# Kernel tuning notes

Hardware: AMD Instinct MI355X
Metric: run time of the kernel (lower is better)

## Reference

```python
import jax, jax.numpy as jnp
import numpy as np

B = 1048576  # batch size
EPS_CLAMP_LO = 1e-6
EPS_CLAMP_HI = 1.0 - 1e-6


def _build_mask():
    # mask[k, i, j] = 1 iff i + j == k, flattened to [19, 100]
    i = np.arange(10)
    m = np.zeros((19, 10, 10), dtype=np.float32)
    ii, jj = np.meshgrid(i, i, indexing='ij')
    m[(ii + jj).ravel(), ii.ravel(), jj.ravel()] = 1.0
    return jnp.asarray(m.reshape(19, 100))


def setup_inputs() -> dict:
    key = jax.random.key(0)
    k1, k2, k3, k4 = jax.random.split(key, 4)
    # concept probabilities: uniform then normalize rows to sum 1
    p1 = jax.random.uniform(k1, (B, 10), dtype=jnp.float32)
    p1 = p1 / p1.sum(axis=1, keepdims=True)
    p2 = jax.random.uniform(k2, (B, 10), dtype=jnp.float32)
    p2 = p2 / p2.sum(axis=1, keepdims=True)
    # learnable permutation-tree weights (binaryTreeLogicNet leaf maps)
    W1 = jax.random.uniform(k3, (10, 10), dtype=jnp.float32)
    W2 = jax.random.uniform(k4, (10, 10), dtype=jnp.float32)
    mask = _build_mask()
    return {"p1": p1, "p2": p2, "W1": W1, "W2": W2, "mask": mask}


def _minmax_norm(W):
    lo = W.min(axis=1, keepdims=True)
    hi = W.max(axis=1, keepdims=True)
    return (W - lo) / (hi - lo + 1e-8)


def reference(p1, p2, W1, W2, mask):
    # input_to_leaf: learned soft permutation with minmax-normalized weights
    p1p = p1 @ _minmax_norm(W1)                      # [B,10]
    p2p = p2 @ _minmax_norm(W2)                      # [B,10]
    # MinMaxAggregator graded AND at andness=1.0 -> elementwise min over all pairs
    s = jnp.minimum(p1p[:, :, None], p2p[:, None, :])  # [B,10,10]
    one_minus = 1.0 - jnp.clip(s, EPS_CLAMP_LO, EPS_CLAMP_HI)
    log_one_minus = jnp.log(one_minus + 1e-12).reshape(-1, 100)  # [B,100]
    # fused masked reduction over all 19 sum bins: [B,100] @ [100,19]
    log_prod = log_one_minus @ mask.T                # [B,19]
    y_prob = 1.0 - jnp.exp(log_prod)                 # smooth OR per sum class
    y_prob = y_prob / (y_prob.sum(axis=1, keepdims=True) + 1e-9)
    return y_prob
```

## Files before the change

kernel.cpp:

```cpp
#include <hip/hip_runtime.h>


#define NBLOCKS 4096

__global__ __launch_bounds__(256) void bacon_main(
    const float* __restrict__ p1, const float* __restrict__ p2,
    const float* __restrict__ W1, const float* __restrict__ W2,
    float* __restrict__ out)
{
    __shared__ __align__(16) float s_out[4864];
    __shared__ __align__(16) float s_w[240];

    const int t = threadIdx.x;
    const int blk = blockIdx.x;

    float a[10], b[10];
    {
        const float2* g1 = (const float2*)p1 + (size_t)blk * 1280 + t * 5;
        const float2* g2 = (const float2*)p2 + (size_t)blk * 1280 + t * 5;
        #pragma unroll
        for (int e = 0; e < 5; ++e) {
            float2 v1 = g1[e];
            float2 v2 = g2[e];
            a[2 * e] = v1.x; a[2 * e + 1] = v1.y;
            b[2 * e] = v2.x; b[2 * e + 1] = v2.y;
        }
    }

    if (t < 20) {
        const float* row = ((t < 10) ? W1 : W2) + (t % 10) * 10;
        float r[10];
        #pragma unroll
        for (int i = 0; i < 10; ++i) r[i] = row[i];
        float lo = r[0], hi = r[0];
        #pragma unroll
        for (int i = 1; i < 10; ++i) {
            lo = fminf(lo, r[i]);
            hi = fmaxf(hi, r[i]);
        }
        float inv = 1.0f / (hi - lo + 1e-8f);
        float* o = s_w + ((t < 10) ? 0 : 120) + (t % 10) * 12;
        #pragma unroll
        for (int i = 0; i < 10; ++i) o[i] = (r[i] - lo) * inv;
        o[10] = 0.0f; o[11] = 0.0f;
    }
    __syncthreads();

    float A[10], Bv[10];
    #pragma unroll
    for (int i = 0; i < 10; ++i) { A[i] = 1.0f; Bv[i] = 1.0f; }
    #pragma unroll
    for (int k = 0; k < 10; ++k) {
        float ak = a[k], bk = b[k];
        const float4* w1q = (const float4*)(s_w + k * 12);
        const float4* w2q = (const float4*)(s_w + 120 + k * 12);
        float4 u0 = w1q[0], u1 = w1q[1];
        float2 u2 = *(const float2*)(s_w + k * 12 + 8);
        float4 v0 = w2q[0], v1 = w2q[1];
        float2 v2 = *(const float2*)(s_w + 120 + k * 12 + 8);
        A[0] = fmaf(-ak, u0.x, A[0]); A[1] = fmaf(-ak, u0.y, A[1]);
        A[2] = fmaf(-ak, u0.z, A[2]); A[3] = fmaf(-ak, u0.w, A[3]);
        A[4] = fmaf(-ak, u1.x, A[4]); A[5] = fmaf(-ak, u1.y, A[5]);
        A[6] = fmaf(-ak, u1.z, A[6]); A[7] = fmaf(-ak, u1.w, A[7]);
        A[8] = fmaf(-ak, u2.x, A[8]); A[9] = fmaf(-ak, u2.y, A[9]);
        Bv[0] = fmaf(-bk, v0.x, Bv[0]); Bv[1] = fmaf(-bk, v0.y, Bv[1]);
        Bv[2] = fmaf(-bk, v0.z, Bv[2]); Bv[3] = fmaf(-bk, v0.w, Bv[3]);
        Bv[4] = fmaf(-bk, v1.x, Bv[4]); Bv[5] = fmaf(-bk, v1.y, Bv[5]);
        Bv[6] = fmaf(-bk, v1.z, Bv[6]); Bv[7] = fmaf(-bk, v1.w, Bv[7]);
        Bv[8] = fmaf(-bk, v2.x, Bv[8]); Bv[9] = fmaf(-bk, v2.y, Bv[9]);
    }

    float prod[19];
    #pragma unroll
    for (int k = 0; k < 19; ++k) prod[k] = 1.0f;
    #pragma unroll
    for (int i = 0; i < 10; ++i) {
        #pragma unroll
        for (int j = 0; j < 10; ++j) {
            prod[i + j] *= fmaxf(A[i], Bv[j]);
        }
    }

    float y[19];
    float tot = 0.0f;
    #pragma unroll
    for (int k = 0; k < 19; ++k) { y[k] = 1.0f - prod[k]; tot += y[k]; }
    float inv = __builtin_amdgcn_rcpf(tot + 1e-9f);

    #pragma unroll
    for (int k = 0; k < 19; ++k) s_out[t * 19 + k] = y[k] * inv;
    __syncthreads();

    {
        const float4* so = (const float4*)s_out;
        float4* go = (float4*)(out + (size_t)blk * 4864);
        #pragma unroll
        for (int it = 0; it < 5; ++it) {
            int idx = t + it * 256;
            if (idx < 1216) go[idx] = so[idx];
        }
    }
}

extern "C" void kernel_launch(void* const* d_in, const int* in_sizes, int n_in,
                              void* d_out, int out_size, void* d_ws, size_t ws_size,
                              hipStream_t stream) {
    const float* p1 = (const float*)d_in[0];
    const float* p2 = (const float*)d_in[1];
    const float* W1 = (const float*)d_in[2];
    const float* W2 = (const float*)d_in[3];
    bacon_main<<<NBLOCKS, 256, 0, stream>>>(p1, p2, W1, W2, (float*)d_out);
}
```

Baseline: 151.4 us.

## Process four row panels per block with register prefetch and double-buffered output

Each block now handles four 256-row panels instead of one, so the grid shrinks to 1024 blocks. The next panel's p1/p2 rows are prefetched into registers while the current panel is computed. Output staging in shared memory is double-buffered so the next panel can proceed with a single barrier per panel. This aims to hide load latency and amortize block launch and weight normalization, at the cost of more registers, more LDS, and fewer blocks available to fill the GPU.

```diff
diff --git a/kernel.cpp b/kernel.cpp
--- a/kernel.cpp
+++ b/kernel.cpp
@@ -1,30 +1,27 @@
 #include <hip/hip_runtime.h>
 
 
-#define NBLOCKS 4096
+#define NBLOCKS 1024
+#define PANELS 4
 
-__global__ __launch_bounds__(256) void bacon_main(
+__global__ __launch_bounds__(256, 4) void bacon_main(
     const float* __restrict__ p1, const float* __restrict__ p2,
     const float* __restrict__ W1, const float* __restrict__ W2,
     float* __restrict__ out)
 {
-    __shared__ __align__(16) float s_out[4864];
+    __shared__ __align__(16) float s_out[2][4864];
     __shared__ __align__(16) float s_w[240];
 
     const int t = threadIdx.x;
     const int blk = blockIdx.x;
+    const size_t row0 = (size_t)blk * (256 * PANELS) + t;
 
-    float a[10], b[10];
+    float2 va[2][5], vb[2][5];
     {
-        const float2* g1 = (const float2*)p1 + (size_t)blk * 1280 + t * 5;
-        const float2* g2 = (const float2*)p2 + (size_t)blk * 1280 + t * 5;
+        const float2* g1 = (const float2*)(p1 + row0 * 10);
+        const float2* g2 = (const float2*)(p2 + row0 * 10);
         #pragma unroll
-        for (int e = 0; e < 5; ++e) {
-            float2 v1 = g1[e];
-            float2 v2 = g2[e];
-            a[2 * e] = v1.x; a[2 * e + 1] = v1.y;
-            b[2 * e] = v2.x; b[2 * e + 1] = v2.y;
-        }
+        for (int e = 0; e < 5; ++e) { va[0][e] = g1[e]; vb[0][e] = g2[e]; }
     }
 
     if (t < 20) {
@@ -46,58 +43,72 @@
     }
     __syncthreads();
 
-    float A[10], Bv[10];
     #pragma unroll
-    for (int i = 0; i < 10; ++i) { A[i] = 1.0f; Bv[i] = 1.0f; }
-    #pragma unroll
-    for (int k = 0; k < 10; ++k) {
-        float ak = a[k], bk = b[k];
-        const float4* w1q = (const float4*)(s_w + k * 12);
-        const float4* w2q = (const float4*)(s_w + 120 + k * 12);
-        float4 u0 = w1q[0], u1 = w1q[1];
-        float2 u2 = *(const float2*)(s_w + k * 12 + 8);
-        float4 v0 = w2q[0], v1 = w2q[1];
-        float2 v2 = *(const float2*)(s_w + 120 + k * 12 + 8);
-        A[0] = fmaf(-ak, u0.x, A[0]); A[1] = fmaf(-ak, u0.y, A[1]);
-        A[2] = fmaf(-ak, u0.z, A[2]); A[3] = fmaf(-ak, u0.w, A[3]);
-        A[4] = fmaf(-ak, u1.x, A[4]); A[5] = fmaf(-ak, u1.y, A[5]);
-        A[6] = fmaf(-ak, u1.z, A[6]); A[7] = fmaf(-ak, u1.w, A[7]);
-        A[8] = fmaf(-ak, u2.x, A[8]); A[9] = fmaf(-ak, u2.y, A[9]);
-        Bv[0] = fmaf(-bk, v0.x, Bv[0]); Bv[1] = fmaf(-bk, v0.y, Bv[1]);
-        Bv[2] = fmaf(-bk, v0.z, Bv[2]); Bv[3] = fmaf(-bk, v0.w, Bv[3]);
-        Bv[4] = fmaf(-bk, v1.x, Bv[4]); Bv[5] = fmaf(-bk, v1.y, Bv[5]);
-        Bv[6] = fmaf(-bk, v1.z, Bv[6]); Bv[7] = fmaf(-bk, v1.w, Bv[7]);
-        Bv[8] = fmaf(-bk, v2.x, Bv[8]); Bv[9] = fmaf(-bk, v2.y, Bv[9]);
-    }
+    for (int p = 0; p < PANELS; ++p) {
+        const int cur = p & 1;
 
-    float prod[19];
-    #pragma unroll
-    for (int k = 0; k < 19; ++k) prod[k] = 1.0f;
-    #pragma unroll
-    for (int i = 0; i < 10; ++i) {
+        if (p + 1 < PANELS) {
+            const int nxt = cur ^ 1;
+            const float2* g1 = (const float2*)(p1 + (row0 + (size_t)(p + 1) * 256) * 10);
+            const float2* g2 = (const float2*)(p2 + (row0 + (size_t)(p + 1) * 256) * 10);
+            #pragma unroll
+            for (int e = 0; e < 5; ++e) { va[nxt][e] = g1[e]; vb[nxt][e] = g2[e]; }
+        }
+
+        float A[10], Bv[10];
         #pragma unroll
-        for (int j = 0; j < 10; ++j) {
-            prod[i + j] *= fmaxf(A[i], Bv[j]);
+        for (int i = 0; i < 10; ++i) { A[i] = 1.0f; Bv[i] = 1.0f; }
+        #pragma unroll
+        for (int k = 0; k < 10; ++k) {
+            const float ak = (k & 1) ? va[cur][k >> 1].y : va[cur][k >> 1].x;
+            const float bk = (k & 1) ? vb[cur][k >> 1].y : vb[cur][k >> 1].x;
+            const float4* w1q = (const float4*)(s_w + k * 12);
+            const float4* w2q = (const float4*)(s_w + 120 + k * 12);
+            float4 u0 = w1q[0], u1 = w1q[1];
+            float2 u2 = *(const float2*)(s_w + k * 12 + 8);
+            float4 v0 = w2q[0], v1 = w2q[1];
+            float2 v2 = *(const float2*)(s_w + 120 + k * 12 + 8);
+            A[0] = fmaf(-ak, u0.x, A[0]); A[1] = fmaf(-ak, u0.y, A[1]);
+            A[2] = fmaf(-ak, u0.z, A[2]); A[3] = fmaf(-ak, u0.w, A[3]);
+            A[4] = fmaf(-ak, u1.x, A[4]); A[5] = fmaf(-ak, u1.y, A[5]);
+            A[6] = fmaf(-ak, u1.z, A[6]); A[7] = fmaf(-ak, u1.w, A[7]);
+            A[8] = fmaf(-ak, u2.x, A[8]); A[9] = fmaf(-ak, u2.y, A[9]);
+            Bv[0] = fmaf(-bk, v0.x, Bv[0]); Bv[1] = fmaf(-bk, v0.y, Bv[1]);
+            Bv[2] = fmaf(-bk, v0.z, Bv[2]); Bv[3] = fmaf(-bk, v0.w, Bv[3]);
+            Bv[4] = fmaf(-bk, v1.x, Bv[4]); Bv[5] = fmaf(-bk, v1.y, Bv[5]);
+            Bv[6] = fmaf(-bk, v1.z, Bv[6]); Bv[7] = fmaf(-bk, v1.w, Bv[7]);
+            Bv[8] = fmaf(-bk, v2.x, Bv[8]); Bv[9] = fmaf(-bk, v2.y, Bv[9]);
         }
-    }
 
-    float y[19];
-    float tot = 0.0f;
-    #pragma unroll
-    for (int k = 0; k < 19; ++k) { y[k] = 1.0f - prod[k]; tot += y[k]; }
-    float inv = __builtin_amdgcn_rcpf(tot + 1e-9f);
+        float prod[19];
+        #pragma unroll
+        for (int k = 0; k < 19; ++k) prod[k] = 1.0f;
+        #pragma unroll
+        for (int i = 0; i < 10; ++i) {
+            #pragma unroll
+            for (int j = 0; j < 10; ++j) {
+                prod[i + j] *= fmaxf(A[i], Bv[j]);
+            }
+        }
 
-    #pragma unroll
-    for (int k = 0; k < 19; ++k) s_out[t * 19 + k] = y[k] * inv;
-    __syncthreads();
+        float y[19];
+        float tot = 0.0f;
+        #pragma unroll
+        for (int k = 0; k < 19; ++k) { y[k] = 1.0f - prod[k]; tot += y[k]; }
+        float invn = __builtin_amdgcn_rcpf(tot + 1e-9f);
 
-    {
-        const float4* so = (const float4*)s_out;
-        float4* go = (float4*)(out + (size_t)blk * 4864);
         #pragma unroll
-        for (int it = 0; it < 5; ++it) {
-            int idx = t + it * 256;
-            if (idx < 1216) go[idx] = so[idx];
+        for (int k = 0; k < 19; ++k) s_out[cur][t * 19 + k] = y[k] * invn;
+        __syncthreads();
+
+        {
+            const float4* so = (const float4*)s_out[cur];
+            float4* go = (float4*)(out + ((size_t)blk * PANELS + p) * 4864);
+            #pragma unroll
+            for (int it = 0; it < 5; ++it) {
+                int idx = t + it * 256;
+                if (idx < 1216) go[idx] = so[idx];
+            }
         }
     }
 }
```

New measurement: 154.0 us. About the same (+1.7%).
